# Kernel tuning notes

Measured on AMD Instinct MI355X. Metric: run time of the kernel, lower is better.

## Reference

```python
import jax, jax.numpy as jnp
import numpy as np

SEQ, IN_DIM, OUT_DIM = 8192, 1024, 1024

def setup_inputs() -> dict:
    key = jax.random.key(0)
    k1, k2, k3, k4 = jax.random.split(key, 4)
    inputs = jax.random.normal(k1, (SEQ, IN_DIM), dtype=jnp.float32)
    # torch.nn.Linear stores weight as [out_dim, in_dim]; y = x @ W.T
    w_query = jax.random.normal(k2, (OUT_DIM, IN_DIM), dtype=jnp.float32) * (1.0 / np.sqrt(IN_DIM))
    w_key = jax.random.normal(k3, (OUT_DIM, IN_DIM), dtype=jnp.float32) * (1.0 / np.sqrt(IN_DIM))
    w_value = jax.random.normal(k4, (OUT_DIM, IN_DIM), dtype=jnp.float32) * (1.0 / np.sqrt(IN_DIM))
    return {"inputs": inputs, "w_query": w_query, "w_key": w_key, "w_value": w_value}

def reference(inputs, w_query, w_key, w_value):
    # QKV projections: [S, D_out]
    q = inputs @ w_query.T
    k = inputs @ w_key.T
    v = inputs @ w_value.T
    scale = 1.0 / jnp.sqrt(jnp.asarray(k.shape[-1], dtype=q.dtype))
    scores = (q @ k.T) * scale  # [S, S]
    # causal mask: lower-triangular kept, upper set to -inf
    s = scores.shape[0]
    causal = jnp.tril(jnp.ones((s, s), dtype=bool))
    scores = jnp.where(causal, scores, -jnp.inf)
    attn = jax.nn.softmax(scores, axis=-1)
    return attn @ v
```

## Files before the change

### kernel.cpp

```cpp
#include <hip/hip_runtime.h>
#include <stdint.h>
#include <stddef.h>


#define SEQ   8192
#define DIM   1024

typedef __bf16 bf16x8 __attribute__((ext_vector_type(8)));
typedef float  f32x4  __attribute__((ext_vector_type(4)));

#define MFMA16(a, b, c) __builtin_amdgcn_mfma_f32_16x16x32_bf16((a), (b), (c), 0, 0, 0)

__device__ __forceinline__ uint16_t f2bf(float f) {
  uint32_t u = __builtin_bit_cast(uint32_t, f);
  return (uint16_t)((u + 0x7fffu + ((u >> 16) & 1u)) >> 16);
}
__device__ __forceinline__ float bf2f(uint16_t h) {
  uint32_t u = ((uint32_t)h) << 16;
  return __builtin_bit_cast(float, u);
}

typedef const __attribute__((address_space(1))) uint32_t* gas_t;
typedef __attribute__((address_space(3))) uint32_t* las_t;
__device__ __forceinline__ void async16(const void* g, void* l) {
  __builtin_amdgcn_global_load_lds((gas_t)g, (las_t)l, 16, 0, 0);
}

__global__ __launch_bounds__(256) void cast_all(const float* __restrict__ x,
                                                const float* __restrict__ wq,
                                                const float* __restrict__ wk,
                                                const float* __restrict__ wv,
                                                uint16_t* __restrict__ xb,
                                                uint16_t* __restrict__ wcat) {
  int b = blockIdx.x;
  const float* src;
  uint16_t* dst;
  int i;
  if (b < 8192) {
    src = x; dst = xb; i = (b * 256 + threadIdx.x) * 4;
  } else {
    int wb = b - 8192;
    int sel = wb >> 10;
    src = sel == 0 ? wq : (sel == 1 ? wk : wv);
    dst = wcat + sel * 1048576;
    i = ((wb & 1023) * 256 + threadIdx.x) * 4;
  }
  float4 v = *(const float4*)(src + i);
  ushort4 o;
  o.x = f2bf(v.x); o.y = f2bf(v.y); o.z = f2bf(v.z); o.w = f2bf(v.w);
  *(ushort4*)(dst + i) = o;
}

__global__ __launch_bounds__(256) void qkv_gemm(const uint16_t* __restrict__ A,
                                                const uint16_t* __restrict__ B,
                                                uint16_t* __restrict__ Qblk,
                                                uint16_t* __restrict__ Kblk,
                                                uint16_t* __restrict__ Vblk) {
  __shared__ __align__(16) uint16_t As[128 * 64];
  __shared__ __align__(16) uint16_t Bs[128 * 64];
  const int t    = threadIdx.x;
  const int w    = t >> 6;
  const int lane = t & 63;
  const int lm   = lane & 15;
  const int qd   = lane >> 4;
  const int wrow = (w >> 1) * 64;
  const int wcol = (w & 1) * 64;
  const int rowbase = blockIdx.y * 128;
  const int colbase = blockIdx.x * 128;

  const int lrow = lane >> 3;
  const int lgrp = (lane & 7) ^ (lrow & 7);

  f32x4 acc[4][4] = {};

  for (int kb = 0; kb < DIM; kb += 64) {
    __syncthreads();
#pragma unroll
    for (int rep = 0; rep < 4; ++rep) {
      int r0 = rep * 32 + w * 8;
      async16(A + (size_t)(rowbase + r0 + lrow) * DIM + kb + lgrp * 8, As + r0 * 64);
      async16(B + (size_t)(colbase + r0 + lrow) * DIM + kb + lgrp * 8, Bs + r0 * 64);
    }
    __syncthreads();
#pragma unroll
    for (int kc = 0; kc < 2; ++kc) {
      bf16x8 af[4], bfr[4];
#pragma unroll
      for (int mt = 0; mt < 4; ++mt) {
        int r = wrow + mt * 16 + lm;
        af[mt] = *(const bf16x8*)(As + r * 64 + (((kc * 4 + qd) ^ (lm & 7)) * 8));
      }
#pragma unroll
      for (int nt = 0; nt < 4; ++nt) {
        int r = wcol + nt * 16 + lm;
        bfr[nt] = *(const bf16x8*)(Bs + r * 64 + (((kc * 4 + qd) ^ (lm & 7)) * 8));
      }
#pragma unroll
      for (int mt = 0; mt < 4; ++mt)
#pragma unroll
        for (int nt = 0; nt < 4; ++nt)
          acc[mt][nt] = MFMA16(af[mt], bfr[nt], acc[mt][nt]);
    }
  }

#pragma unroll
  for (int mt = 0; mt < 4; ++mt)
#pragma unroll
    for (int nt = 0; nt < 4; ++nt)
#pragma unroll
      for (int r = 0; r < 4; ++r) {
        int m = rowbase + wrow + mt * 16 + qd * 4 + r;
        int n = colbase + wcol + nt * 16 + lm;
        uint16_t v = f2bf(acc[mt][nt][r]);
        int nn = n & 1023;
        if (n < 2048) {
          size_t off = (((size_t)(m >> 4) * 32 + (nn >> 5)) * 64 +
                        ((nn >> 3) & 3) * 16 + (m & 15)) * 8 + (nn & 7);
          if (n < 1024) Qblk[off] = v; else Kblk[off] = v;
        } else {
          size_t off = (((size_t)(nn >> 4) * 256 + (m >> 5)) * 64 +
                        ((m >> 3) & 3) * 16 + (nn & 15)) * 8 + (m & 7);
          Vblk[off] = v;
        }
      }
}

__global__ __launch_bounds__(1024) void attn_kernel(const uint16_t* __restrict__ Qblk,
                                                    const uint16_t* __restrict__ Kblk,
                                                    const uint16_t* __restrict__ Vblk,
                                                    uint16_t* __restrict__ P0,
                                                    uint16_t* __restrict__ P1,
                                                    float* __restrict__ Mm,
                                                    float* __restrict__ Ll) {
  __shared__ __align__(16) uint16_t Qs[32768];
  __shared__ __align__(16) uint16_t Pb[8192];
  __shared__ float stats[32][16];
  __shared__ float mrow[32];

  const int t    = threadIdx.x;
  const int w    = t >> 6;
  const int lane = t & 63;
  const int lm   = lane & 15;
  const int qd   = lane >> 4;
  const int slot = blockIdx.x >> 3;
  const int p    = (blockIdx.x & 7) * 16 + (slot >> 1);
  const int par  = slot & 1;
  const float c1 = 0.045084220027780106f;

#pragma unroll 1
  for (int half = 0; half < 2; ++half) {
    const int tt   = half ? 255 - p : p;
    const int row0 = tt * 32;
    const int jn   = (tt >> 3) + 1;

    __syncthreads();
#pragma unroll
    for (int i = 0; i < 4; ++i)
      async16(Qblk + ((size_t)(tt * 64 + w * 4 + i)) * 512 + lane * 8,
              Qs + (w * 4 + i) * 512);
    __syncthreads();

    float m_run[2][4], l_run[2][4];
#pragma unroll
    for (int mt = 0; mt < 2; ++mt)
#pragma unroll
      for (int r = 0; r < 4; ++r) { m_run[mt][r] = -1e30f; l_run[mt][r] = 0.0f; }
    f32x4 o_acc[2][4] = {};

#pragma unroll 1
    for (int jg = par; jg < jn; jg += 2) {
      const uint16_t* kbp = Kblk + ((size_t)(jg * 16 + w) * 32) * 512 + lane * 8;
      const uint16_t* vbp = Vblk + ((size_t)(w * 4) * 256 + jg * 8) * 512 + lane * 8;
      const uint16_t* qsp = Qs + lane * 8;

      f32x4 sacc[2] = {};
      bf16x8 kr[4];
#pragma unroll
      for (int c = 0; c < 4; ++c)
        kr[c] = *(const bf16x8*)(kbp + (size_t)c * 512);
#pragma unroll
      for (int kb = 0; kb < 32; ++kb) {
        bf16x8 q0 = *(const bf16x8*)(qsp + kb * 512);
        bf16x8 q1 = *(const bf16x8*)(qsp + (32 + kb) * 512);
        bf16x8 kcur = kr[kb & 3];
        if (kb < 28)
          kr[kb & 3] = *(const bf16x8*)(kbp + (size_t)(kb + 4) * 512);
        sacc[0] = MFMA16(q0, kcur, sacc[0]);
        sacc[1] = MFMA16(q1, kcur, sacc[1]);
      }

      if (jg == jn - 1) {
#pragma unroll
        for (int mt = 0; mt < 2; ++mt)
#pragma unroll
          for (int r = 0; r < 4; ++r) {
            int col = jg * 256 + w * 16 + lm;
            int row = row0 + mt * 16 + qd * 4 + r;
            if (col > row) sacc[mt][r] = -1e30f;
          }
      }

#pragma unroll
      for (int mt = 0; mt < 2; ++mt)
#pragma unroll
        for (int r = 0; r < 4; ++r) {
          float v = sacc[mt][r];
          v = fmaxf(v, __shfl_xor(v, 1));
          v = fmaxf(v, __shfl_xor(v, 2));
          v = fmaxf(v, __shfl_xor(v, 4));
          v = fmaxf(v, __shfl_xor(v, 8));
          if (lm == 0) stats[mt * 16 + qd * 4 + r][w] = v;
        }
      __syncthreads();

      bf16x8 vr[4];
#pragma unroll
      for (int u = 0; u < 4; ++u)
        vr[u] = *(const bf16x8*)(vbp + ((size_t)(u >> 3) * 256 + (u & 7)) * 512);

      float alpha[2][4], psum[2][4];
#pragma unroll
      for (int mt = 0; mt < 2; ++mt)
#pragma unroll
        for (int r = 0; r < 4; ++r) {
          int rl = mt * 16 + qd * 4 + r;
          float4 g0 = *(const float4*)&stats[rl][0];
          float4 g1 = *(const float4*)&stats[rl][4];
          float4 g2 = *(const float4*)&stats[rl][8];
          float4 g3 = *(const float4*)&stats[rl][12];
          float gm = fmaxf(
              fmaxf(fmaxf(fmaxf(g0.x, g0.y), fmaxf(g0.z, g0.w)),
                    fmaxf(fmaxf(g1.x, g1.y), fmaxf(g1.z, g1.w))),
              fmaxf(fmaxf(fmaxf(g2.x, g2.y), fmaxf(g2.z, g2.w)),
                    fmaxf(fmaxf(g3.x, g3.y), fmaxf(g3.z, g3.w))));
          float mn = fmaxf(m_run[mt][r], gm);
          alpha[mt][r] = exp2f((m_run[mt][r] - mn) * c1);
          m_run[mt][r] = mn;
          psum[mt][r] = 0.0f;
        }
#pragma unroll
      for (int mt = 0; mt < 2; ++mt)
#pragma unroll
        for (int r = 0; r < 4; ++r) {
          float pv = exp2f((sacc[mt][r] - m_run[mt][r]) * c1);
          psum[mt][r] += pv;
          Pb[((mt * 8 + (w >> 1)) * 64 + ((w & 1) * 2 + (lm >> 3)) * 16 +
              qd * 4 + r) * 8 + (lm & 7)] = f2bf(pv);
        }
#pragma unroll
      for (int mt = 0; mt < 2; ++mt)
#pragma unroll
        for (int r = 0; r < 4; ++r) {
          float s2 = psum[mt][r];
          s2 += __shfl_xor(s2, 1);
          s2 += __shfl_xor(s2, 2);
          s2 += __shfl_xor(s2, 4);
          s2 += __shfl_xor(s2, 8);
          l_run[mt][r] = l_run[mt][r] * alpha[mt][r] + s2;
        }
      __syncthreads();

#pragma unroll
      for (int mt = 0; mt < 2; ++mt)
#pragma unroll
        for (int dt = 0; dt < 4; ++dt)
#pragma unroll
          for (int r = 0; r < 4; ++r)
            o_acc[mt][dt][r] *= alpha[mt][r];

#pragma unroll
      for (int u = 0; u < 32; ++u) {
        const int dt = u >> 3, kc = u & 7;
        bf16x8 pf0 = *(const bf16x8*)(Pb + (kc * 64 + lane) * 8);
        bf16x8 pf1 = *(const bf16x8*)(Pb + ((8 + kc) * 64 + lane) * 8);
        bf16x8 vf = vr[u & 3];
        if (u < 28)
          vr[u & 3] = *(const bf16x8*)(vbp +
              ((size_t)((u + 4) >> 3) * 256 + ((u + 4) & 7)) * 512);
        o_acc[0][dt] = MFMA16(pf0, vf, o_acc[0][dt]);
        o_acc[1][dt] = MFMA16(pf1, vf, o_acc[1][dt]);
      }
    }

    if (lm == 0) {
#pragma unroll
      for (int mt = 0; mt < 2; ++mt)
#pragma unroll
        for (int r = 0; r < 4; ++r) {
          int rl = mt * 16 + qd * 4 + r;
          stats[rl][w] = l_run[mt][r];
          if (w == 0) mrow[rl] = m_run[mt][r];
        }
    }
    __syncthreads();
    if (t < 32) {
      float4 a0 = *(const float4*)&stats[t][0];
      float4 a1 = *(const float4*)&stats[t][4];
      float4 a2 = *(const float4*)&stats[t][8];
      float4 a3 = *(const float4*)&stats[t][12];
      Mm[par * SEQ + row0 + t] = mrow[t];
      Ll[par * SEQ + row0 + t] = (a0.x + a0.y + a0.z + a0.w) +
                                 (a1.x + a1.y + a1.z + a1.w) +
                                 (a2.x + a2.y + a2.z + a2.w) +
                                 (a3.x + a3.y + a3.z + a3.w);
    }
    uint16_t* Pp = par ? P1 : P0;
#pragma unroll
    for (int mt = 0; mt < 2; ++mt)
#pragma unroll
      for (int dt = 0; dt < 4; ++dt)
#pragma unroll
        for (int r = 0; r < 4; ++r) {
          int row = row0 + mt * 16 + qd * 4 + r;
          int d   = w * 64 + dt * 16 + lm;
          Pp[(size_t)row * DIM + d] = f2bf(o_acc[mt][dt][r]);
        }
  }
}

__global__ __launch_bounds__(256) void merge_kernel(const uint16_t* __restrict__ P0,
                                                    const uint16_t* __restrict__ P1,
                                                    const float* __restrict__ Mm,
                                                    const float* __restrict__ Ll,
                                                    float* __restrict__ out) {
  const int row = blockIdx.x;
  const int d0  = threadIdx.x * 4;
  const float c1 = 0.045084220027780106f;
  float m0 = Mm[row], m1 = Mm[SEQ + row];
  float l0 = Ll[row], l1 = Ll[SEQ + row];
  float m  = fmaxf(m0, m1);
  float a0 = exp2f((m0 - m) * c1);
  float a1 = exp2f((m1 - m) * c1);
  float inv = 1.0f / (a0 * l0 + a1 * l1);
  ushort4 p0 = *(const ushort4*)(P0 + (size_t)row * DIM + d0);
  ushort4 p1 = *(const ushort4*)(P1 + (size_t)row * DIM + d0);
  float4 o;
  o.x = (a0 * bf2f(p0.x) + a1 * bf2f(p1.x)) * inv;
  o.y = (a0 * bf2f(p0.y) + a1 * bf2f(p1.y)) * inv;
  o.z = (a0 * bf2f(p0.z) + a1 * bf2f(p1.z)) * inv;
  o.w = (a0 * bf2f(p0.w) + a1 * bf2f(p1.w)) * inv;
  *(float4*)(out + (size_t)row * DIM + d0) = o;
}

extern "C" void kernel_launch(void* const* d_in, const int* in_sizes, int n_in,
                              void* d_out, int out_size, void* d_ws, size_t ws_size,
                              hipStream_t stream) {
  (void)in_sizes; (void)n_in; (void)out_size; (void)ws_size;
  const float* x  = (const float*)d_in[0];
  const float* wq = (const float*)d_in[1];
  const float* wk = (const float*)d_in[2];
  const float* wv = (const float*)d_in[3];
  float* out = (float*)d_out;

  char* ws = (char*)d_ws;
  uint16_t* Qblk = (uint16_t*)(ws);
  uint16_t* Kblk = (uint16_t*)(ws + 16777216);
  uint16_t* Vblk = (uint16_t*)(ws + 33554432);
  uint16_t* P0   = (uint16_t*)(ws + 50331648);
  uint16_t* xb   = (uint16_t*)(ws + 67108864);
  uint16_t* P1   = (uint16_t*)(ws + 67108864);
  uint16_t* wcat = (uint16_t*)(ws + 83886080);
  float*    Mm   = (float*)(ws + 83886080);
  float*    Ll   = (float*)(ws + 83886080 + 65536);

  cast_all<<<11264, 256, 0, stream>>>(x, wq, wk, wv, xb, wcat);
  qkv_gemm<<<dim3(24, 64), 256, 0, stream>>>(xb, wcat, Qblk, Kblk, Vblk);
  attn_kernel<<<256, 1024, 0, stream>>>(Qblk, Kblk, Vblk, P0, P1, Mm, Ll);
  merge_kernel<<<SEQ, 256, 0, stream>>>(P0, P1, Mm, Ll, out);
}
```

Measured before the change: 502.9 us.

## Split attention into 512 smaller blocks with 128-key tiles per 8 waves

```diff
diff --git a/kernel.cpp b/kernel.cpp
--- a/kernel.cpp
+++ b/kernel.cpp
@@ -125,16 +125,16 @@
       }
 }
 
-__global__ __launch_bounds__(1024) void attn_kernel(const uint16_t* __restrict__ Qblk,
-                                                    const uint16_t* __restrict__ Kblk,
-                                                    const uint16_t* __restrict__ Vblk,
-                                                    uint16_t* __restrict__ P0,
-                                                    uint16_t* __restrict__ P1,
-                                                    float* __restrict__ Mm,
-                                                    float* __restrict__ Ll) {
+__global__ __launch_bounds__(512, 4) void attn_kernel(const uint16_t* __restrict__ Qblk,
+                                                      const uint16_t* __restrict__ Kblk,
+                                                      const uint16_t* __restrict__ Vblk,
+                                                      uint16_t* __restrict__ P0,
+                                                      uint16_t* __restrict__ P1,
+                                                      float* __restrict__ Mm,
+                                                      float* __restrict__ Ll) {
   __shared__ __align__(16) uint16_t Qs[32768];
-  __shared__ __align__(16) uint16_t Pb[8192];
-  __shared__ float stats[32][16];
+  __shared__ __align__(16) uint16_t Pb[4096];
+  __shared__ float stats[32][8];
   __shared__ float mrow[32];
 
   const int t    = threadIdx.x;
@@ -142,180 +142,168 @@
   const int lane = t & 63;
   const int lm   = lane & 15;
   const int qd   = lane >> 4;
-  const int slot = blockIdx.x >> 3;
-  const int p    = (blockIdx.x & 7) * 16 + (slot >> 1);
-  const int par  = slot & 1;
+  const int b    = blockIdx.x;
+  const int s    = b >> 3;
+  const int q2   = s >> 1;
+  const int par  = q2 & 1;
+  const int pi   = (b & 7) * 16 + (q2 >> 1);
+  const int tt   = (s & 1) ? 255 - pi : pi;
+  const int row0 = tt * 32;
+  const int jn   = (tt >> 2) + 1;
   const float c1 = 0.045084220027780106f;
 
+#pragma unroll
+  for (int i = 0; i < 8; ++i)
+    async16(Qblk + ((size_t)(tt * 64 + w * 8 + i)) * 512 + lane * 8,
+            Qs + (w * 8 + i) * 512);
+  __syncthreads();
+
+  float m_run[2][4], l_run[2][4];
+#pragma unroll
+  for (int mt = 0; mt < 2; ++mt)
+#pragma unroll
+    for (int r = 0; r < 4; ++r) { m_run[mt][r] = -1e30f; l_run[mt][r] = 0.0f; }
+  f32x4 o_acc[2][8] = {};
+
 #pragma unroll 1
-  for (int half = 0; half < 2; ++half) {
-    const int tt   = half ? 255 - p : p;
-    const int row0 = tt * 32;
-    const int jn   = (tt >> 3) + 1;
-
+  for (int jg = par; jg < jn; jg += 2) {
+    const uint16_t* kbp = Kblk + ((size_t)(jg * 8 + w) * 32) * 512 + lane * 8;
+    const uint16_t* vbp = Vblk + ((size_t)(w * 8) * 256 + jg * 4) * 512 + lane * 8;
+    const uint16_t* qsp = Qs + lane * 8;
+
+    f32x4 sacc[2] = {};
+    bf16x8 kr[4];
+#pragma unroll
+    for (int c = 0; c < 4; ++c)
+      kr[c] = *(const bf16x8*)(kbp + (size_t)c * 512);
+#pragma unroll
+    for (int kb = 0; kb < 32; ++kb) {
+      bf16x8 q0 = *(const bf16x8*)(qsp + kb * 512);
+      bf16x8 q1 = *(const bf16x8*)(qsp + (32 + kb) * 512);
+      bf16x8 kcur = kr[kb & 3];
+      if (kb < 28)
+        kr[kb & 3] = *(const bf16x8*)(kbp + (size_t)(kb + 4) * 512);
+      sacc[0] = MFMA16(q0, kcur, sacc[0]);
+      sacc[1] = MFMA16(q1, kcur, sacc[1]);
+    }
+
+    if (jg == jn - 1) {
+#pragma unroll
+      for (int mt = 0; mt < 2; ++mt)
+#pragma unroll
+        for (int r = 0; r < 4; ++r) {
+          int col = jg * 128 + w * 16 + lm;
+          int row = row0 + mt * 16 + qd * 4 + r;
+          if (col > row) sacc[mt][r] = -1e30f;
+        }
+    }
+
+#pragma unroll
+    for (int mt = 0; mt < 2; ++mt)
+#pragma unroll
+      for (int r = 0; r < 4; ++r) {
+        float v = sacc[mt][r];
+        v = fmaxf(v, __shfl_xor(v, 1));
+        v = fmaxf(v, __shfl_xor(v, 2));
+        v = fmaxf(v, __shfl_xor(v, 4));
+        v = fmaxf(v, __shfl_xor(v, 8));
+        if (lm == 0) stats[mt * 16 + qd * 4 + r][w] = v;
+      }
     __syncthreads();
-#pragma unroll
-    for (int i = 0; i < 4; ++i)
-      async16(Qblk + ((size_t)(tt * 64 + w * 4 + i)) * 512 + lane * 8,
-              Qs + (w * 4 + i) * 512);
+
+    bf16x8 vr[4];
+#pragma unroll
+    for (int u = 0; u < 4; ++u)
+      vr[u] = *(const bf16x8*)(vbp + ((size_t)(u >> 2) * 256 + (u & 3)) * 512);
+
+    float alpha[2][4], psum[2][4];
+#pragma unroll
+    for (int mt = 0; mt < 2; ++mt)
+#pragma unroll
+      for (int r = 0; r < 4; ++r) {
+        int rl = mt * 16 + qd * 4 + r;
+        float4 g0 = *(const float4*)&stats[rl][0];
+        float4 g1 = *(const float4*)&stats[rl][4];
+        float gm = fmaxf(fmaxf(fmaxf(g0.x, g0.y), fmaxf(g0.z, g0.w)),
+                         fmaxf(fmaxf(g1.x, g1.y), fmaxf(g1.z, g1.w)));
+        float mn = fmaxf(m_run[mt][r], gm);
+        alpha[mt][r] = exp2f((m_run[mt][r] - mn) * c1);
+        m_run[mt][r] = mn;
+        psum[mt][r] = 0.0f;
+      }
+#pragma unroll
+    for (int mt = 0; mt < 2; ++mt)
+#pragma unroll
+      for (int r = 0; r < 4; ++r) {
+        float pv = exp2f((sacc[mt][r] - m_run[mt][r]) * c1);
+        psum[mt][r] += pv;
+        Pb[((mt * 4 + (w >> 1)) * 64 + ((w & 1) * 2 + (lm >> 3)) * 16 +
+            qd * 4 + r) * 8 + (lm & 7)] = f2bf(pv);
+      }
+#pragma unroll
+    for (int mt = 0; mt < 2; ++mt)
+#pragma unroll
+      for (int r = 0; r < 4; ++r) {
+        float s2 = psum[mt][r];
+        s2 += __shfl_xor(s2, 1);
+        s2 += __shfl_xor(s2, 2);
+        s2 += __shfl_xor(s2, 4);
+        s2 += __shfl_xor(s2, 8);
+        l_run[mt][r] = l_run[mt][r] * alpha[mt][r] + s2;
+      }
     __syncthreads();
 
-    float m_run[2][4], l_run[2][4];
-#pragma unroll
-    for (int mt = 0; mt < 2; ++mt)
-#pragma unroll
-      for (int r = 0; r < 4; ++r) { m_run[mt][r] = -1e30f; l_run[mt][r] = 0.0f; }
-    f32x4 o_acc[2][4] = {};
-
-#pragma unroll 1
-    for (int jg = par; jg < jn; jg += 2) {
-      const uint16_t* kbp = Kblk + ((size_t)(jg * 16 + w) * 32) * 512 + lane * 8;
-      const uint16_t* vbp = Vblk + ((size_t)(w * 4) * 256 + jg * 8) * 512 + lane * 8;
-      const uint16_t* qsp = Qs + lane * 8;
-
-      f32x4 sacc[2] = {};
-      bf16x8 kr[4];
-#pragma unroll
-      for (int c = 0; c < 4; ++c)
-        kr[c] = *(const bf16x8*)(kbp + (size_t)c * 512);
-#pragma unroll
-      for (int kb = 0; kb < 32; ++kb) {
-        bf16x8 q0 = *(const bf16x8*)(qsp + kb * 512);
-        bf16x8 q1 = *(const bf16x8*)(qsp + (32 + kb) * 512);
-        bf16x8 kcur = kr[kb & 3];
-        if (kb < 28)
-          kr[kb & 3] = *(const bf16x8*)(kbp + (size_t)(kb + 4) * 512);
-        sacc[0] = MFMA16(q0, kcur, sacc[0]);
-        sacc[1] = MFMA16(q1, kcur, sacc[1]);
-      }
-
-      if (jg == jn - 1) {
-#pragma unroll
-        for (int mt = 0; mt < 2; ++mt)
-#pragma unroll
-          for (int r = 0; r < 4; ++r) {
-            int col = jg * 256 + w * 16 + lm;
-            int row = row0 + mt * 16 + qd * 4 + r;
-            if (col > row) sacc[mt][r] = -1e30f;
-          }
-      }
-
-#pragma unroll
-      for (int mt = 0; mt < 2; ++mt)
-#pragma unroll
-        for (int r = 0; r < 4; ++r) {
-          float v = sacc[mt][r];
-          v = fmaxf(v, __shfl_xor(v, 1));
-          v = fmaxf(v, __shfl_xor(v, 2));
-          v = fmaxf(v, __shfl_xor(v, 4));
-          v = fmaxf(v, __shfl_xor(v, 8));
-          if (lm == 0) stats[mt * 16 + qd * 4 + r][w] = v;
-        }
-      __syncthreads();
-
-      bf16x8 vr[4];
-#pragma unroll
-      for (int u = 0; u < 4; ++u)
-        vr[u] = *(const bf16x8*)(vbp + ((size_t)(u >> 3) * 256 + (u & 7)) * 512);
-
-      float alpha[2][4], psum[2][4];
-#pragma unroll
-      for (int mt = 0; mt < 2; ++mt)
-#pragma unroll
-        for (int r = 0; r < 4; ++r) {
-          int rl = mt * 16 + qd * 4 + r;
-          float4 g0 = *(const float4*)&stats[rl][0];
-          float4 g1 = *(const float4*)&stats[rl][4];
-          float4 g2 = *(const float4*)&stats[rl][8];
-          float4 g3 = *(const float4*)&stats[rl][12];
-          float gm = fmaxf(
-              fmaxf(fmaxf(fmaxf(g0.x, g0.y), fmaxf(g0.z, g0.w)),
-                    fmaxf(fmaxf(g1.x, g1.y), fmaxf(g1.z, g1.w))),
-              fmaxf(fmaxf(fmaxf(g2.x, g2.y), fmaxf(g2.z, g2.w)),
-                    fmaxf(fmaxf(g3.x, g3.y), fmaxf(g3.z, g3.w))));
-          float mn = fmaxf(m_run[mt][r], gm);
-          alpha[mt][r] = exp2f((m_run[mt][r] - mn) * c1);
-          m_run[mt][r] = mn;
-          psum[mt][r] = 0.0f;
-        }
-#pragma unroll
-      for (int mt = 0; mt < 2; ++mt)
-#pragma unroll
-        for (int r = 0; r < 4; ++r) {
-          float pv = exp2f((sacc[mt][r] - m_run[mt][r]) * c1);
-          psum[mt][r] += pv;
-          Pb[((mt * 8 + (w >> 1)) * 64 + ((w & 1) * 2 + (lm >> 3)) * 16 +
-              qd * 4 + r) * 8 + (lm & 7)] = f2bf(pv);
-        }
-#pragma unroll
-      for (int mt = 0; mt < 2; ++mt)
-#pragma unroll
-        for (int r = 0; r < 4; ++r) {
-          float s2 = psum[mt][r];
-          s2 += __shfl_xor(s2, 1);
-          s2 += __shfl_xor(s2, 2);
-          s2 += __shfl_xor(s2, 4);
-          s2 += __shfl_xor(s2, 8);
-          l_run[mt][r] = l_run[mt][r] * alpha[mt][r] + s2;
-        }
-      __syncthreads();
-
-#pragma unroll
-      for (int mt = 0; mt < 2; ++mt)
-#pragma unroll
-        for (int dt = 0; dt < 4; ++dt)
-#pragma unroll
-          for (int r = 0; r < 4; ++r)
-            o_acc[mt][dt][r] *= alpha[mt][r];
-
-#pragma unroll
-      for (int u = 0; u < 32; ++u) {
-        const int dt = u >> 3, kc = u & 7;
-        bf16x8 pf0 = *(const bf16x8*)(Pb + (kc * 64 + lane) * 8);
-        bf16x8 pf1 = *(const bf16x8*)(Pb + ((8 + kc) * 64 + lane) * 8);
-        bf16x8 vf = vr[u & 3];
-        if (u < 28)
-          vr[u & 3] = *(const bf16x8*)(vbp +
-              ((size_t)((u + 4) >> 3) * 256 + ((u + 4) & 7)) * 512);
-        o_acc[0][dt] = MFMA16(pf0, vf, o_acc[0][dt]);
-        o_acc[1][dt] = MFMA16(pf1, vf, o_acc[1][dt]);
-      }
-    }
-
-    if (lm == 0) {
-#pragma unroll
-      for (int mt = 0; mt < 2; ++mt)
-#pragma unroll
-        for (int r = 0; r < 4; ++r) {
-          int rl = mt * 16 + qd * 4 + r;
-          stats[rl][w] = l_run[mt][r];
-          if (w == 0) mrow[rl] = m_run[mt][r];
-        }
-    }
-    __syncthreads();
-    if (t < 32) {
-      float4 a0 = *(const float4*)&stats[t][0];
-      float4 a1 = *(const float4*)&stats[t][4];
-      float4 a2 = *(const float4*)&stats[t][8];
-      float4 a3 = *(const float4*)&stats[t][12];
-      Mm[par * SEQ + row0 + t] = mrow[t];
-      Ll[par * SEQ + row0 + t] = (a0.x + a0.y + a0.z + a0.w) +
-                                 (a1.x + a1.y + a1.z + a1.w) +
-                                 (a2.x + a2.y + a2.z + a2.w) +
-                                 (a3.x + a3.y + a3.z + a3.w);
-    }
-    uint16_t* Pp = par ? P1 : P0;
-#pragma unroll
-    for (int mt = 0; mt < 2; ++mt)
-#pragma unroll
-      for (int dt = 0; dt < 4; ++dt)
-#pragma unroll
-        for (int r = 0; r < 4; ++r) {
-          int row = row0 + mt * 16 + qd * 4 + r;
-          int d   = w * 64 + dt * 16 + lm;
-          Pp[(size_t)row * DIM + d] = f2bf(o_acc[mt][dt][r]);
-        }
-  }
+#pragma unroll
+    for (int mt = 0; mt < 2; ++mt)
+#pragma unroll
+      for (int dt = 0; dt < 8; ++dt)
+#pragma unroll
+        for (int r = 0; r < 4; ++r)
+          o_acc[mt][dt][r] *= alpha[mt][r];
+
+#pragma unroll
+    for (int u = 0; u < 32; ++u) {
+      const int dt = u >> 2, kc = u & 3;
+      bf16x8 pf0 = *(const bf16x8*)(Pb + ((0 * 4 + kc) * 64 + lane) * 8);
+      bf16x8 pf1 = *(const bf16x8*)(Pb + ((1 * 4 + kc) * 64 + lane) * 8);
+      bf16x8 vf = vr[u & 3];
+      if (u < 28)
+        vr[u & 3] = *(const bf16x8*)(vbp +
+            ((size_t)((u + 4) >> 2) * 256 + ((u + 4) & 3)) * 512);
+      o_acc[0][dt] = MFMA16(pf0, vf, o_acc[0][dt]);
+      o_acc[1][dt] = MFMA16(pf1, vf, o_acc[1][dt]);
+    }
+  }
+
+  if (lm == 0) {
+#pragma unroll
+    for (int mt = 0; mt < 2; ++mt)
+#pragma unroll
+      for (int r = 0; r < 4; ++r) {
+        int rl = mt * 16 + qd * 4 + r;
+        stats[rl][w] = l_run[mt][r];
+        if (w == 0) mrow[rl] = m_run[mt][r];
+      }
+  }
+  __syncthreads();
+  if (t < 32) {
+    float4 a0 = *(const float4*)&stats[t][0];
+    float4 a1 = *(const float4*)&stats[t][4];
+    Mm[par * SEQ + row0 + t] = mrow[t];
+    Ll[par * SEQ + row0 + t] = (a0.x + a0.y + a0.z + a0.w) +
+                               (a1.x + a1.y + a1.z + a1.w);
+  }
+  uint16_t* Pp = par ? P1 : P0;
+#pragma unroll
+  for (int mt = 0; mt < 2; ++mt)
+#pragma unroll
+    for (int dt = 0; dt < 8; ++dt)
+#pragma unroll
+      for (int r = 0; r < 4; ++r) {
+        int row = row0 + mt * 16 + qd * 4 + r;
+        int d   = w * 128 + dt * 16 + lm;
+        Pp[(size_t)row * DIM + d] = f2bf(o_acc[mt][dt][r]);
+      }
 }
 
 __global__ __launch_bounds__(256) void merge_kernel(const uint16_t* __restrict__ P0,
@@ -365,6 +353,6 @@
 
   cast_all<<<11264, 256, 0, stream>>>(x, wq, wk, wv, xb, wcat);
   qkv_gemm<<<dim3(24, 64), 256, 0, stream>>>(xb, wcat, Qblk, Kblk, Vblk);
-  attn_kernel<<<256, 1024, 0, stream>>>(Qblk, Kblk, Vblk, P0, P1, Mm, Ll);
+  attn_kernel<<<512, 512, 0, stream>>>(Qblk, Kblk, Vblk, P0, P1, Mm, Ll);
   merge_kernel<<<SEQ, 256, 0, stream>>>(P0, P1, Mm, Ll, out);
 }
```

New measurement: 910.7 us. 81.1% more time.
